# Kernel tuning notes

Measured on AMD Instinct MI355X. Metric: run time of the kernel, lower is better.

## Reference

```python
import jax, jax.numpy as jnp
import numpy as np

B, N, L, E, H, D = 2, 2048, 2048, 512, 8, 3
C = E // H
ALPHA_Q = 10.0

def _ln(v, g, b):
    m = jnp.mean(v, -1, keepdims=True)
    var = jnp.mean((v - m) ** 2, -1, keepdims=True)
    return (v - m) * jax.lax.rsqrt(var + 1e-5) * g + b

def setup_inputs() -> dict:
    key = jax.random.key(0)
    ks = jax.random.split(key, 16)
    def nrm(k, shape):
        return jax.random.normal(k, shape, jnp.float32) * 0.02
    return dict(
        x=jax.random.normal(ks[0], (B, N, E), jnp.float32),
        xp=jax.random.normal(ks[1], (B, N, D), jnp.float32),
        y=jax.random.normal(ks[2], (B, L, E), jnp.float32),
        yp=jax.random.normal(ks[3], (B, L, D), jnp.float32),
        attn_mask=jnp.ones((B, 1, N, L), jnp.float32),
        pW1=jax.random.uniform(ks[4], (E, D), jnp.float32, -1.0 / D, 1.0 / D),
        pb1=jax.random.uniform(ks[5], (E,), jnp.float32, 0.0, np.pi),
        pW2=jax.random.uniform(ks[6], (E, D), jnp.float32, -1.0 / D, 1.0 / D),
        pb2=jax.random.uniform(ks[7], (E,), jnp.float32, 0.0, np.pi),
        qn_g=jnp.ones((E,), jnp.float32), qn_b=jnp.zeros((E,), jnp.float32),
        qW1=nrm(ks[8], (E, E)), qb1=jnp.zeros((E,), jnp.float32),
        qW2=nrm(ks[9], (E, E)), qb2=jnp.zeros((E,), jnp.float32),
        kn_g=jnp.ones((E,), jnp.float32), kn_b=jnp.zeros((E,), jnp.float32),
        kW1=nrm(ks[10], (E, E)), kb1=jnp.zeros((E,), jnp.float32),
        vn_g=jnp.ones((E,), jnp.float32), vn_b=jnp.zeros((E,), jnp.float32),
        vW=nrm(ks[11], (E, E)), vb=jnp.zeros((E,), jnp.float32),
        p1W=nrm(ks[12], (E, E)), p1b=jnp.zeros((E,), jnp.float32),
        p2W=nrm(ks[13], (E, D * H)), p2b=jnp.zeros((E,), jnp.float32),
    )

def reference(x, xp, y, yp, attn_mask, pW1, pb1, pW2, pb2,
              qn_g, qn_b, qW1, qb1, qW2, qb2, kn_g, kn_b, kW1, kb1,
              vn_g, vn_b, vW, vb, p1W, p1b, p2W, p2b):
    # PositionEncoder: query side with bias, key side without
    pxs = ALPHA_Q * xp
    px1 = pxs @ pW1.T + pb1
    px2 = pxs @ pW2.T + pb2
    xc1, xs1, xc2, xs2 = jnp.cos(px1), jnp.sin(px1), jnp.cos(px2), jnp.sin(px2)
    pys = ALPHA_Q * yp
    py1 = pys @ pW1.T
    py2 = pys @ pW2.T
    yc1, ys1, yc2, ys2 = jnp.cos(py1), jnp.sin(py1), jnp.cos(py2), jnp.sin(py2)

    def split(t):  # [B,S,E] -> [B,S,H,C]
        return t.reshape(t.shape[0], t.shape[1], H, C)

    # QueryEncoder
    xn = _ln(x, qn_g, qn_b)
    x1 = xn @ qW1.T + qb1
    x2 = xn @ qW2.T + qb2
    q = jnp.concatenate([split(x1 * xc1), split(x1 * xs1),
                         split(x2 * xc2), split(x2 * xs2)], -1)  # [B,N,H,4C]
    q = q.transpose(0, 2, 1, 3)  # [B,H,N,4C]
    # KeyEncoder
    yn = _ln(y, kn_g, kn_b)
    y1 = yn @ kW1.T + kb1
    k = jnp.concatenate([split(y1 * yc1), split(y1 * ys1),
                         split(yc2), split(ys2)], -1).transpose(0, 2, 1, 3)

    scale = (4 * C) ** -0.5
    attn = jax.nn.softmax(jnp.einsum('bhnd,bhld->bhnl', q, k) * scale, axis=-1)
    # custom mask renormalization
    attn = attn * attn_mask
    eps = min(1e-8, 1.0 / L)
    attn = attn / (jnp.sum(attn, -1, keepdims=True) + eps)

    v = (_ln(y, vn_g, vn_b) @ vW.T + vb).reshape(B, L, H, C).transpose(0, 2, 1, 3)
    out1 = jnp.einsum('bhnl,bhlc->bhnc', attn, v).transpose(0, 2, 1, 3).reshape(B, N, E)
    out1 = out1 @ p1W.T + p1b

    out2 = jnp.einsum('bhnl,bld->bhnd', attn, yp) - xp[:, None]  # [B,H,N,D]
    out2 = out2.transpose(0, 2, 1, 3).reshape(B, N, H * D) @ p2W.T + p2b
    return (out1 + out2, attn)
```

## Files before the change

kernel.cpp:

```cpp
#include <hip/hip_runtime.h>

typedef unsigned short ushort_t;
typedef __attribute__((ext_vector_type(8))) __bf16 bf16x8;
typedef __attribute__((ext_vector_type(4))) float f32x4;

__device__ __forceinline__ f32x4 mfma16(bf16x8 a, bf16x8 b, f32x4 c) {
  return __builtin_amdgcn_mfma_f32_16x16x32_bf16(a, b, c, 0, 0, 0);
}

__device__ __forceinline__ ushort_t f2bf(float f) {
  unsigned int x = __float_as_uint(f);
  unsigned int r = (x + 0x7fffu + ((x >> 16) & 1u)) >> 16;
  return (ushort_t)r;
}

static constexpr size_t SZ_XN   = 4096ull * 512 * 2;
static constexpr size_t SZ_W    = 512ull * 512 * 2;
static constexpr size_t OFS_XN   = 0;
static constexpr size_t OFS_YNK  = OFS_XN + SZ_XN;
static constexpr size_t OFS_YNV  = OFS_YNK + SZ_XN;
static constexpr size_t OFS_WQ12 = OFS_YNV + SZ_XN;
static constexpr size_t OFS_WK1  = OFS_WQ12 + 2 * SZ_W;
static constexpr size_t OFS_WV   = OFS_WK1 + SZ_W;
static constexpr size_t OFS_WP1  = OFS_WV + SZ_W;
static constexpr size_t OFS_QB12 = OFS_WP1 + SZ_W;
static constexpr size_t OFS_FLAG = OFS_QB12 + 4096;
static constexpr size_t OFS_X12  = OFS_FLAG + 256;
static constexpr size_t OFS_Y1   = OFS_X12 + 4096ull * 1024 * 4;
static constexpr size_t OFS_VV   = OFS_Y1 + 4096ull * 512 * 4;
static constexpr size_t OFS_Q    = OFS_VV + 4096ull * 512 * 4;
static constexpr size_t OFS_K    = OFS_Q + 16ull * 2048 * 256 * 2;
static constexpr size_t OFS_VT   = OFS_K + 16ull * 2048 * 256 * 2;
static constexpr size_t OFS_O1   = OFS_VT + 16ull * 80 * 2048 * 2;
static constexpr size_t OFS_O2   = OFS_O1 + 4096ull * 512 * 2;

__global__ void k_convert(const float* __restrict__ qW1, const float* __restrict__ qW2,
                          const float* __restrict__ kW1, const float* __restrict__ vW,
                          const float* __restrict__ p1W,
                          const float* __restrict__ qb1, const float* __restrict__ qb2,
                          ushort_t* wq12, ushort_t* wk1, ushort_t* wv, ushort_t* wp1,
                          float* qb12, int* flag) {
  int seg = blockIdx.y;
  int idx = blockIdx.x * 256 + threadIdx.x;
  switch (seg) {
    case 0: wq12[idx] = f2bf(qW1[idx]);
            if (idx < 512) qb12[idx] = qb1[idx];
            if (idx == 0) *flag = 1;
            break;
    case 1: wq12[262144 + idx] = f2bf(qW2[idx]);
            if (idx < 512) qb12[512 + idx] = qb2[idx];
            break;
    case 2: wk1[idx] = f2bf(kW1[idx]); break;
    case 3: wv[idx]  = f2bf(vW[idx]);  break;
    case 4: wp1[idx] = f2bf(p1W[idx]); break;
  }
}

__global__ void k_maskchk(const float4* __restrict__ mask, int* flag, int n4) {
  int i = blockIdx.x * blockDim.x + threadIdx.x;
  bool bad = false;
  for (; i < n4; i += gridDim.x * blockDim.x) {
    float4 v = mask[i];
    bad |= (v.x != 1.f) | (v.y != 1.f) | (v.z != 1.f) | (v.w != 1.f);
  }
  if (bad) atomicAnd(flag, 0);
}

__global__ __launch_bounds__(256) void k_ln1(const float* __restrict__ x,
                                             const float* __restrict__ g, const float* __restrict__ b,
                                             ushort_t* __restrict__ out) {
  int row = blockIdx.x, tid = threadIdx.x;
  const float* xr = x + (size_t)row * 512;
  float v0 = xr[tid], v1 = xr[tid + 256];
  float s = v0 + v1, q = v0 * v0 + v1 * v1;
  for (int m = 32; m; m >>= 1) { s += __shfl_xor(s, m, 64); q += __shfl_xor(q, m, 64); }
  __shared__ float ls[8];
  int wid = tid >> 6, lane = tid & 63;
  if (lane == 0) { ls[wid] = s; ls[4 + wid] = q; }
  __syncthreads();
  s = ls[0] + ls[1] + ls[2] + ls[3];
  q = ls[4] + ls[5] + ls[6] + ls[7];
  float mean = s * (1.f / 512), var = q * (1.f / 512) - mean * mean;
  float rs = rsqrtf(var + 1e-5f);
  ushort_t* o = out + (size_t)row * 512;
  o[tid]       = f2bf((v0 - mean) * rs * g[tid] + b[tid]);
  o[tid + 256] = f2bf((v1 - mean) * rs * g[tid + 256] + b[tid + 256]);
}

__global__ __launch_bounds__(256) void k_ln2(const float* __restrict__ y,
                                             const float* __restrict__ g1, const float* __restrict__ b1,
                                             const float* __restrict__ g2, const float* __restrict__ b2,
                                             ushort_t* __restrict__ o1, ushort_t* __restrict__ o2) {
  int row = blockIdx.x, tid = threadIdx.x;
  const float* yr = y + (size_t)row * 512;
  float v0 = yr[tid], v1 = yr[tid + 256];
  float s = v0 + v1, q = v0 * v0 + v1 * v1;
  for (int m = 32; m; m >>= 1) { s += __shfl_xor(s, m, 64); q += __shfl_xor(q, m, 64); }
  __shared__ float ls[8];
  int wid = tid >> 6, lane = tid & 63;
  if (lane == 0) { ls[wid] = s; ls[4 + wid] = q; }
  __syncthreads();
  s = ls[0] + ls[1] + ls[2] + ls[3];
  q = ls[4] + ls[5] + ls[6] + ls[7];
  float mean = s * (1.f / 512), var = q * (1.f / 512) - mean * mean;
  float rs = rsqrtf(var + 1e-5f);
  float t0 = (v0 - mean) * rs, t1 = (v1 - mean) * rs;
  ushort_t* p1 = o1 + (size_t)row * 512;
  ushort_t* p2 = o2 + (size_t)row * 512;
  p1[tid]       = f2bf(t0 * g1[tid] + b1[tid]);
  p1[tid + 256] = f2bf(t1 * g1[tid + 256] + b1[tid + 256]);
  p2[tid]       = f2bf(t0 * g2[tid] + b2[tid]);
  p2[tid + 256] = f2bf(t1 * g2[tid + 256] + b2[tid + 256]);
}

__global__ __launch_bounds__(256) void k_gemm(const ushort_t* __restrict__ A, const ushort_t* __restrict__ W,
                                              const float* __restrict__ bias, float* __restrict__ Cmat,
                                              int M, int Nn, int K, int mode,
// ... 57 lines not shown
}

__global__ __launch_bounds__(256) void k_scatter_q(const float* __restrict__ x12, const float* __restrict__ xp,
                                                   const float* __restrict__ pW1, const float* __restrict__ pb1,
                                                   const float* __restrict__ pW2, const float* __restrict__ pb2,
                                                   ushort_t* __restrict__ q) {
  int rown = blockIdx.x;
  int b = rown >> 11, n = rown & 2047;
  float p0 = xp[(size_t)rown * 3] * 10.f;
  float p1 = xp[(size_t)rown * 3 + 1] * 10.f;
  float p2v = xp[(size_t)rown * 3 + 2] * 10.f;
  const float* x1r = x12 + (size_t)rown * 1024;
#pragma unroll
  for (int i = 0; i < 2; i++) {
    int e = threadIdx.x + i * 256;
    float a1 = p0 * pW1[e * 3] + p1 * pW1[e * 3 + 1] + p2v * pW1[e * 3 + 2] + pb1[e];
    float a2 = p0 * pW2[e * 3] + p1 * pW2[e * 3 + 1] + p2v * pW2[e * 3 + 2] + pb2[e];
    float c1, s1, c2, s2;
    __sincosf(a1, &s1, &c1);
    __sincosf(a2, &s2, &c2);
    float x1 = x1r[e], x2 = x1r[512 + e];
    int h = e >> 6, c = e & 63;
    ushort_t* qr = q + (((size_t)b * 8 + h) * 2048 + n) * 256;
    qr[c]       = f2bf(x1 * c1);
    qr[64 + c]  = f2bf(x1 * s1);
    qr[128 + c] = f2bf(x2 * c2);
    qr[192 + c] = f2bf(x2 * s2);
  }
}

__global__ __launch_bounds__(256) void k_scatter_k(const float* __restrict__ y1, const float* __restrict__ yp,
                                                   const float* __restrict__ pW1, const float* __restrict__ pW2,
                                                   ushort_t* __restrict__ kk) {
  int rown = blockIdx.x;
  int b = rown >> 11, n = rown & 2047;
  float p0 = yp[(size_t)rown * 3] * 10.f;
  float p1 = yp[(size_t)rown * 3 + 1] * 10.f;
  float p2v = yp[(size_t)rown * 3 + 2] * 10.f;
  const float* y1r = y1 + (size_t)rown * 512;
#pragma unroll
  for (int i = 0; i < 2; i++) {
    int e = threadIdx.x + i * 256;
    float a1 = p0 * pW1[e * 3] + p1 * pW1[e * 3 + 1] + p2v * pW1[e * 3 + 2];
    float a2 = p0 * pW2[e * 3] + p1 * pW2[e * 3 + 1] + p2v * pW2[e * 3 + 2];
    float c1, s1, c2, s2;
    __sincosf(a1, &s1, &c1);
    __sincosf(a2, &s2, &c2);
    float v1 = y1r[e];
    int h = e >> 6, c = e & 63;
    ushort_t* kr = kk + (((size_t)b * 8 + h) * 2048 + n) * 256;
    kr[c]       = f2bf(v1 * c1);
    kr[64 + c]  = f2bf(v1 * s1);
    kr[128 + c] = f2bf(c2);
    kr[192 + c] = f2bf(s2);
  }
}

__global__ void k_vt(const float* __restrict__ vv, ushort_t* __restrict__ vt) {
  int l0 = blockIdx.x * 64, h = blockIdx.y, b = blockIdx.z;
  __shared__ ushort_t t[64][66];
  int tx = threadIdx.x, ty = threadIdx.y;
#pragma unroll
  for (int i = 0; i < 16; i++) {
    int lr = i * 4 + ty;
    t[lr][tx] = f2bf(vv[((size_t)(b * 2048 + l0 + lr)) * 512 + h * 64 + tx]);
  }
  __syncthreads();
#pragma unroll
  for (int i = 0; i < 16; i++) {
    int col = i * 4 + ty;
    vt[(((size_t)b * 8 + h) * 80 + col) * 2048 + l0 + tx] = t[tx][col];
  }
}

__global__ void k_vt_extra(const float* __restrict__ yp, ushort_t* __restrict__ vt) {
  int l = blockIdx.x * 256 + threadIdx.x;
  int j = blockIdx.y, bh = blockIdx.z;
  int b = bh >> 3;
  ushort_t v = 0;
  if (j < 3) v = f2bf(yp[((size_t)b * 2048 + l) * 3 + j]);
  vt[((size_t)bh * 80 + 64 + j) * 2048 + l] = v;
}

__global__ __launch_bounds__(256, 2) void k_attn(const ushort_t* __restrict__ qbuf,
                                                 const ushort_t* __restrict__ kbuf,
                                                 const ushort_t* __restrict__ vt,
                                                 const float* __restrict__ mask,
                                                 const int* __restrict__ flag,
                                                 const float* __restrict__ xp,
                                                 float* __restrict__ attn_out,
                                                 ushort_t* __restrict__ o1,
                                                 float* __restrict__ o2) {
  __shared__ __align__(16) ushort_t kL[2][32 * 256];
  __shared__ __align__(16) ushort_t aT[4][16][40];

  int flat = blockIdx.x;
  int bh = flat & 15, rb = flat >> 4;
  int b = bh >> 3, h = bh & 7;
  int tid = threadIdx.x, wid = tid >> 6, lane = tid & 63, lg = lane >> 4, lc = lane & 15;
  int n0 = rb * 64;
  int wrow = n0 + wid * 16;
  const bool ones = (*flag != 0);

  const ushort_t* Kb = kbuf + (size_t)bh * 2048 * 256;
  const ushort_t* Vb = vt + (size_t)bh * 80 * 2048;

  bf16x8 qf[8];
  {
    const ushort_t* qr = qbuf + ((size_t)bh * 2048 + wrow + lc) * 256 + lg * 8;
#pragma unroll
    for (int ks = 0; ks < 8; ks++) qf[ks] = *(const bf16x8*)(qr + ks * 32);
  }

  int sg_src[4], sg_dst[4];
#pragma unroll
  for (int i = 0; i < 4; i++) {
    int g = wid * 256 + i * 64 + lane;
    int row = g >> 5;
    int gc = (g & 31) ^ (row & 7);
    sg_src[i] = row * 256 + gc * 8;
    sg_dst[i] = (wid * 256 + i * 64) * 8;
  }

#define STAGE(s, t)                                                                     \
  {                                                                                     \
    const ushort_t* tb = Kb + (size_t)(t) * 32 * 256;                                   \
    _Pragma("unroll")                                                                   \
    for (int i = 0; i < 4; i++) {                                                       \
      __builtin_amdgcn_global_load_lds(                                                 \
          (const __attribute__((address_space(1))) void*)(tb + sg_src[i]),              \
          (__attribute__((address_space(3))) void*)(&kL[s][sg_dst[i]]), 16, 0, 0);      \
    }                                                                                   \
  }

  int r3 = (lc & 7);

  float rsE[4] = {0, 0, 0, 0}, rsM[4] = {0, 0, 0, 0};
  STAGE(0, 0);
  asm volatile("s_waitcnt vmcnt(0)" ::: "memory");
  __syncthreads();
  for (int t = 0; t < 64; t++) {
    int s = t & 1;
    if (t < 63) { STAGE(s ^ 1, t + 1); }
    __builtin_amdgcn_sched_barrier(0);
    f32x4 sacc[2];
    sacc[0] = (f32x4){0, 0, 0, 0};
    sacc[1] = (f32x4){0, 0, 0, 0};
#pragma unroll
    for (int ks = 0; ks < 8; ks++) {
      int gb = ((ks * 4 + lg) ^ r3) * 8;
      bf16x8 k0 = *(const bf16x8*)(&kL[s][lc * 256 + gb]);
      bf16x8 k1 = *(const bf16x8*)(&kL[s][(16 + lc) * 256 + gb]);
      sacc[0] = mfma16(qf[ks], k0, sacc[0]);
      sacc[1] = mfma16(qf[ks], k1, sacc[1]);
    }
#pragma unroll
    for (int nt = 0; nt < 2; nt++)
#pragma unroll
      for (int r = 0; r < 4; r++) {
        float T = __expf(sacc[nt][r] * 0.0625f);
        rsE[r] += T;
        if (!ones) {
          float m = mask[((size_t)b * 2048 + wrow + lg * 4 + r) * 2048 + t * 32 + nt * 16 + lc];
          rsM[r] += T * m;
        }
      }
    asm volatile("s_waitcnt vmcnt(0)" ::: "memory");
    __syncthreads();
  }

  float inv[4];
#pragma unroll
  for (int r = 0; r < 4; r++) {
#pragma unroll
    for (int s2 = 1; s2 < 16; s2 <<= 1) {
      rsE[r] += __shfl_xor(rsE[r], s2, 64);
      if (!ones) rsM[r] += __shfl_xor(rsM[r], s2, 64);
    }
    float denom = (ones ? rsE[r] : rsM[r]) + 1e-8f * rsE[r];
    inv[r] = 1.f / denom;
  }

  f32x4 pacc[5];
#pragma unroll
  for (int nt = 0; nt < 5; nt++) pacc[nt] = (f32x4){0, 0, 0, 0};

  STAGE(0, 0);
  asm volatile("s_waitcnt vmcnt(0)" ::: "memory");
  __syncthreads();
  for (int t = 0; t < 64; t++) {
    int s = t & 1;
    if (t < 63) { STAGE(s ^ 1, t + 1); }
    __builtin_amdgcn_sched_barrier(0);
    int l0 = t * 32;
    f32x4 sacc[2];
    sacc[0] = (f32x4){0, 0, 0, 0};
    sacc[1] = (f32x4){0, 0, 0, 0};
#pragma unroll
    for (int ks = 0; ks < 8; ks++) {
      int gb = ((ks * 4 + lg) ^ r3) * 8;
      bf16x8 k0 = *(const bf16x8*)(&kL[s][lc * 256 + gb]);
      bf16x8 k1 = *(const bf16x8*)(&kL[s][(16 + lc) * 256 + gb]);
      sacc[0] = mfma16(qf[ks], k0, sacc[0]);
      sacc[1] = mfma16(qf[ks], k1, sacc[1]);
    }
#pragma unroll
    for (int nt = 0; nt < 2; nt++)
#pragma unroll
      for (int r = 0; r < 4; r++) {
        float T = __expf(sacc[nt][r] * 0.0625f);
        float m = 1.f;
        if (!ones) m = mask[((size_t)b * 2048 + wrow + lg * 4 + r) * 2048 + l0 + nt * 16 + lc];
        float a = T * m * inv[r];
        __builtin_nontemporal_store(
            a, &attn_out[((size_t)bh * 2048 + wrow + lg * 4 + r) * 2048 + l0 + nt * 16 + lc]);
        aT[wid][lg * 4 + r][nt * 16 + lc] = f2bf(a);
      }
    asm volatile("s_waitcnt lgkmcnt(0)" ::: "memory");
    __builtin_amdgcn_sched_barrier(0);
    bf16x8 af = *(const bf16x8*)(&aT[wid][lc][lg * 8]);
#pragma unroll
    for (int nt = 0; nt < 5; nt++) {
      bf16x8 vf = *(const bf16x8*)(Vb + (size_t)(nt * 16 + lc) * 2048 + l0 + lg * 8);
      pacc[nt] = mfma16(af, vf, pacc[nt]);
    }
    asm volatile("s_waitcnt vmcnt(8)" ::: "memory");
    __syncthreads();
  }
#undef STAGE

#pragma unroll
  for (int nt = 0; nt < 4; nt++)
#pragma unroll
    for (int r = 0; r < 4; r++) {
      int n = wrow + lg * 4 + r;
      o1[((size_t)b * 2048 + n) * 512 + h * 64 + nt * 16 + lc] = f2bf(pacc[nt][r]);
    }
  if (lc < 3) {
#pragma unroll
    for (int r = 0; r < 4; r++) {
      int n = wrow + lg * 4 + r;
      o2[((size_t)b * 2048 + n) * 24 + h * 3 + lc] = pacc[4][r] - xp[((size_t)b * 2048 + n) * 3 + lc];
    }
  }
}

extern "C" void kernel_launch(void* const* d_in, const int* in_sizes, int n_in,
                              void* d_out, int out_size, void* d_ws, size_t ws_size,
                              hipStream_t stream) {
  const float* x    = (const float*)d_in[0];
  const float* xp   = (const float*)d_in[1];
  const float* y    = (const float*)d_in[2];
  const float* yp   = (const float*)d_in[3];
  const float* mask = (const float*)d_in[4];
  const float* pW1  = (const float*)d_in[5];
  const float* pb1  = (const float*)d_in[6];
  const float* pW2  = (const float*)d_in[7];
  const float* pb2  = (const float*)d_in[8];
  const float* qn_g = (const float*)d_in[9];
  const float* qn_b = (const float*)d_in[10];
  const float* qW1  = (const float*)d_in[11];
  const float* qb1  = (const float*)d_in[12];
  const float* qW2  = (const float*)d_in[13];
  const float* qb2  = (const float*)d_in[14];
  const float* kn_g = (const float*)d_in[15];
  const float* kn_b = (const float*)d_in[16];
  const float* kW1  = (const float*)d_in[17];
  const float* kb1  = (const float*)d_in[18];
  const float* vn_g = (const float*)d_in[19];
  const float* vn_b = (const float*)d_in[20];
  const float* vW   = (const float*)d_in[21];
  const float* vb   = (const float*)d_in[22];
  const float* p1W  = (const float*)d_in[23];
  const float* p1b  = (const float*)d_in[24];
  const float* p2W  = (const float*)d_in[25];
  const float* p2b  = (const float*)d_in[26];

  char* ws = (char*)d_ws;
  ushort_t* xn   = (ushort_t*)(ws + OFS_XN);
  ushort_t* ynk  = (ushort_t*)(ws + OFS_YNK);
  ushort_t* ynv  = (ushort_t*)(ws + OFS_YNV);
  ushort_t* wq12 = (ushort_t*)(ws + OFS_WQ12);
  ushort_t* wk1  = (ushort_t*)(ws + OFS_WK1);
  ushort_t* wv   = (ushort_t*)(ws + OFS_WV);
  ushort_t* wp1  = (ushort_t*)(ws + OFS_WP1);
  float*    qb12 = (float*)(ws + OFS_QB12);
  int*      flag = (int*)(ws + OFS_FLAG);
  float*    x12  = (float*)(ws + OFS_X12);
  float*    y1b  = (float*)(ws + OFS_Y1);
  float*    vvb  = (float*)(ws + OFS_VV);
  ushort_t* qb   = (ushort_t*)(ws + OFS_Q);
  ushort_t* kb   = (ushort_t*)(ws + OFS_K);
  ushort_t* vtb  = (ushort_t*)(ws + OFS_VT);
  ushort_t* o1   = (ushort_t*)(ws + OFS_O1);
  float*    o2   = (float*)(ws + OFS_O2);

  float* out0 = (float*)d_out;
  float* attn_out = (float*)d_out + 2097152;

  k_convert<<<dim3(1024, 5), 256, 0, stream>>>(qW1, qW2, kW1, vW, p1W, qb1, qb2,
                                               wq12, wk1, wv, wp1, qb12, flag);
  k_maskchk<<<2048, 256, 0, stream>>>((const float4*)mask, flag, 2097152);
  k_ln1<<<4096, 256, 0, stream>>>(x, qn_g, qn_b, xn);
  k_ln2<<<4096, 256, 0, stream>>>(y, kn_g, kn_b, vn_g, vn_b, ynk, ynv);
  k_gemm<<<dim3(8, 32), 256, 0, stream>>>(xn, wq12, qb12, x12, 4096, 1024, 512, 0, nullptr, nullptr, nullptr);
  k_gemm<<<dim3(4, 32), 256, 0, stream>>>(ynk, wk1, kb1, y1b, 4096, 512, 512, 0, nullptr, nullptr, nullptr);
  k_gemm<<<dim3(4, 32), 256, 0, stream>>>(ynv, wv, vb, vvb, 4096, 512, 512, 0, nullptr, nullptr, nullptr);
  k_scatter_q<<<4096, 256, 0, stream>>>(x12, xp, pW1, pb1, pW2, pb2, qb);
  k_scatter_k<<<4096, 256, 0, stream>>>(y1b, yp, pW1, pW2, kb);
  k_vt<<<dim3(32, 8, 2), dim3(64, 4), 0, stream>>>(vvb, vtb);
  k_vt_extra<<<dim3(8, 16, 16), 256, 0, stream>>>(yp, vtb);
  k_attn<<<dim3(512), 256, 0, stream>>>(qb, kb, vtb, mask, flag, xp, attn_out, o1, o2);
  k_gemm<<<dim3(4, 32), 256, 0, stream>>>(o1, wp1, p1b, out0, 4096, 512, 512, 1, o2, p2W, p2b);
}
```

Measured before the change: 362.1 us.

## Split attention into single-pass PV kernel and separate attn-matrix writer kernel

The first attention kernel now does one pass over K, accumulating unnormalized probabilities times V and the row sums together, and applies the inverse normalizer at the end. The normalizers go to a workspace buffer. A second kernel recomputes QK^T with register-double-buffered K loads and writes the normalized attention matrix using two 16-row tiles per wave. This removes the duplicate QK pass from the PV kernel and lets the output GEMM run before the large attention write, at the cost of recomputing QK in a separate launch with occupancy 1. The invb buffer reuses the x12 workspace region, which is no longer needed by then.

```diff
diff --git a/kernel.cpp b/kernel.cpp
--- a/kernel.cpp
+++ b/kernel.cpp
@@ -26,6 +26,7 @@
 static constexpr size_t OFS_QB12 = OFS_WP1 + SZ_W;
 static constexpr size_t OFS_FLAG = OFS_QB12 + 4096;
 static constexpr size_t OFS_X12  = OFS_FLAG + 256;
+static constexpr size_t OFS_INV  = OFS_X12;
 static constexpr size_t OFS_Y1   = OFS_X12 + 4096ull * 1024 * 4;
 static constexpr size_t OFS_VV   = OFS_Y1 + 4096ull * 512 * 4;
 static constexpr size_t OFS_Q    = OFS_VV + 4096ull * 512 * 4;
@@ -256,15 +257,15 @@
   vt[((size_t)bh * 80 + 64 + j) * 2048 + l] = v;
 }
 
-__global__ __launch_bounds__(256, 2) void k_attn(const ushort_t* __restrict__ qbuf,
-                                                 const ushort_t* __restrict__ kbuf,
-                                                 const ushort_t* __restrict__ vt,
-                                                 const float* __restrict__ mask,
-                                                 const int* __restrict__ flag,
-                                                 const float* __restrict__ xp,
-                                                 float* __restrict__ attn_out,
-                                                 ushort_t* __restrict__ o1,
-                                                 float* __restrict__ o2) {
+__global__ __launch_bounds__(256, 2) void k_attn1(const ushort_t* __restrict__ qbuf,
+                                                  const ushort_t* __restrict__ kbuf,
+                                                  const ushort_t* __restrict__ vt,
+                                                  const float* __restrict__ mask,
+                                                  const int* __restrict__ flag,
+                                                  const float* __restrict__ xp,
+                                                  float* __restrict__ invb,
+                                                  ushort_t* __restrict__ o1,
+                                                  float* __restrict__ o2) {
   __shared__ __align__(16) ushort_t kL[2][32 * 256];
   __shared__ __align__(16) ushort_t aT[4][16][40];
 
@@ -272,8 +273,7 @@
   int bh = flat & 15, rb = flat >> 4;
   int b = bh >> 3, h = bh & 7;
   int tid = threadIdx.x, wid = tid >> 6, lane = tid & 63, lg = lane >> 4, lc = lane & 15;
-  int n0 = rb * 64;
-  int wrow = n0 + wid * 16;
+  int wrow = rb * 64 + wid * 16;
   const bool ones = (*flag != 0);
 
   const ushort_t* Kb = kbuf + (size_t)bh * 2048 * 256;
@@ -310,12 +310,21 @@
   int r3 = (lc & 7);
 
   float rsE[4] = {0, 0, 0, 0}, rsM[4] = {0, 0, 0, 0};
+  f32x4 pacc[5];
+#pragma unroll
+  for (int nt = 0; nt < 5; nt++) pacc[nt] = (f32x4){0, 0, 0, 0};
+
   STAGE(0, 0);
   asm volatile("s_waitcnt vmcnt(0)" ::: "memory");
   __syncthreads();
   for (int t = 0; t < 64; t++) {
     int s = t & 1;
+    int l0 = t * 32;
     if (t < 63) { STAGE(s ^ 1, t + 1); }
+    bf16x8 vf[5];
+#pragma unroll
+    for (int nt = 0; nt < 5; nt++)
+      vf[nt] = *(const bf16x8*)(Vb + (size_t)(nt * 16 + lc) * 2048 + l0 + lg * 8);
     __builtin_amdgcn_sched_barrier(0);
     f32x4 sacc[2];
     sacc[0] = (f32x4){0, 0, 0, 0};
@@ -334,89 +343,135 @@
       for (int r = 0; r < 4; r++) {
         float T = __expf(sacc[nt][r] * 0.0625f);
         rsE[r] += T;
+        float Tm = T;
         if (!ones) {
-          float m = mask[((size_t)b * 2048 + wrow + lg * 4 + r) * 2048 + t * 32 + nt * 16 + lc];
-          rsM[r] += T * m;
+          float m = mask[((size_t)b * 2048 + wrow + lg * 4 + r) * 2048 + l0 + nt * 16 + lc];
+          Tm = T * m;
+          rsM[r] += Tm;
         }
-      }
-    asm volatile("s_waitcnt vmcnt(0)" ::: "memory");
-    __syncthreads();
-  }
-
-  float inv[4];
-#pragma unroll
-  for (int r = 0; r < 4; r++) {
-#pragma unroll
-    for (int s2 = 1; s2 < 16; s2 <<= 1) {
-      rsE[r] += __shfl_xor(rsE[r], s2, 64);
-      if (!ones) rsM[r] += __shfl_xor(rsM[r], s2, 64);
-    }
-    float denom = (ones ? rsE[r] : rsM[r]) + 1e-8f * rsE[r];
-    inv[r] = 1.f / denom;
-  }
-
-  f32x4 pacc[5];
-#pragma unroll
-  for (int nt = 0; nt < 5; nt++) pacc[nt] = (f32x4){0, 0, 0, 0};
-
-  STAGE(0, 0);
-  asm volatile("s_waitcnt vmcnt(0)" ::: "memory");
-  __syncthreads();
-  for (int t = 0; t < 64; t++) {
-    int s = t & 1;
-    if (t < 63) { STAGE(s ^ 1, t + 1); }
-    __builtin_amdgcn_sched_barrier(0);
-    int l0 = t * 32;
-    f32x4 sacc[2];
-    sacc[0] = (f32x4){0, 0, 0, 0};
-    sacc[1] = (f32x4){0, 0, 0, 0};
-#pragma unroll
-    for (int ks = 0; ks < 8; ks++) {
-      int gb = ((ks * 4 + lg) ^ r3) * 8;
-      bf16x8 k0 = *(const bf16x8*)(&kL[s][lc * 256 + gb]);
-      bf16x8 k1 = *(const bf16x8*)(&kL[s][(16 + lc) * 256 + gb]);
-      sacc[0] = mfma16(qf[ks], k0, sacc[0]);
-      sacc[1] = mfma16(qf[ks], k1, sacc[1]);
-    }
-#pragma unroll
-    for (int nt = 0; nt < 2; nt++)
-#pragma unroll
-      for (int r = 0; r < 4; r++) {
-        float T = __expf(sacc[nt][r] * 0.0625f);
-        float m = 1.f;
-        if (!ones) m = mask[((size_t)b * 2048 + wrow + lg * 4 + r) * 2048 + l0 + nt * 16 + lc];
-        float a = T * m * inv[r];
-        __builtin_nontemporal_store(
-            a, &attn_out[((size_t)bh * 2048 + wrow + lg * 4 + r) * 2048 + l0 + nt * 16 + lc]);
-        aT[wid][lg * 4 + r][nt * 16 + lc] = f2bf(a);
+        aT[wid][lg * 4 + r][nt * 16 + lc] = f2bf(Tm);
       }
     asm volatile("s_waitcnt lgkmcnt(0)" ::: "memory");
     __builtin_amdgcn_sched_barrier(0);
     bf16x8 af = *(const bf16x8*)(&aT[wid][lc][lg * 8]);
 #pragma unroll
-    for (int nt = 0; nt < 5; nt++) {
-      bf16x8 vf = *(const bf16x8*)(Vb + (size_t)(nt * 16 + lc) * 2048 + l0 + lg * 8);
-      pacc[nt] = mfma16(af, vf, pacc[nt]);
-    }
-    asm volatile("s_waitcnt vmcnt(8)" ::: "memory");
+    for (int nt = 0; nt < 5; nt++) pacc[nt] = mfma16(af, vf[nt], pacc[nt]);
     __syncthreads();
   }
 #undef STAGE
+
+  float inv[4];
+#pragma unroll
+  for (int r = 0; r < 4; r++) {
+#pragma unroll
+    for (int s2 = 1; s2 < 16; s2 <<= 1) {
+      rsE[r] += __shfl_xor(rsE[r], s2, 64);
+      if (!ones) rsM[r] += __shfl_xor(rsM[r], s2, 64);
+    }
+    float denom = (ones ? rsE[r] : rsM[r]) + 1e-8f * rsE[r];
+    inv[r] = 1.f / denom;
+  }
+
+  if (lc == 0) {
+#pragma unroll
+    for (int r = 0; r < 4; r++) invb[(size_t)bh * 2048 + wrow + lg * 4 + r] = inv[r];
+  }
 
 #pragma unroll
   for (int nt = 0; nt < 4; nt++)
 #pragma unroll
     for (int r = 0; r < 4; r++) {
       int n = wrow + lg * 4 + r;
-      o1[((size_t)b * 2048 + n) * 512 + h * 64 + nt * 16 + lc] = f2bf(pacc[nt][r]);
+      o1[((size_t)b * 2048 + n) * 512 + h * 64 + nt * 16 + lc] = f2bf(pacc[nt][r] * inv[r]);
     }
   if (lc < 3) {
 #pragma unroll
     for (int r = 0; r < 4; r++) {
       int n = wrow + lg * 4 + r;
-      o2[((size_t)b * 2048 + n) * 24 + h * 3 + lc] = pacc[4][r] - xp[((size_t)b * 2048 + n) * 3 + lc];
-    }
-  }
+      o2[((size_t)b * 2048 + n) * 24 + h * 3 + lc] =
+          pacc[4][r] * inv[r] - xp[((size_t)b * 2048 + n) * 3 + lc];
+    }
+  }
+}
+
+__global__ __launch_bounds__(256, 1) void k_attn2(const ushort_t* __restrict__ qbuf,
+                                                  const ushort_t* __restrict__ kbuf,
+                                                  const float* __restrict__ invb,
+                                                  const float* __restrict__ mask,
+                                                  const int* __restrict__ flag,
+                                                  float* __restrict__ attn_out) {
+  int flat = blockIdx.x;
+  int bh = flat & 15, rb = flat >> 4;
+  int b = bh >> 3;
+  int tid = threadIdx.x, wid = tid >> 6, lane = tid & 63, lg = lane >> 4, lc = lane & 15;
+  int base = rb * 128 + wid * 32;
+  const bool ones = (*flag != 0);
+
+  const ushort_t* Kb = kbuf + (size_t)bh * 2048 * 256;
+  float* aout = attn_out + (size_t)bh * 2048 * 2048;
+
+  bf16x8 qf0[8], qf1[8];
+  {
+    const ushort_t* q0 = qbuf + ((size_t)bh * 2048 + base + lc) * 256 + lg * 8;
+#pragma unroll
+    for (int ks = 0; ks < 8; ks++) {
+      qf0[ks] = *(const bf16x8*)(q0 + ks * 32);
+      qf1[ks] = *(const bf16x8*)(q0 + 16 * 256 + ks * 32);
+    }
+  }
+  float inv0[4], inv1[4];
+#pragma unroll
+  for (int r = 0; r < 4; r++) {
+    inv0[r] = invb[(size_t)bh * 2048 + base + lg * 4 + r];
+    inv1[r] = invb[(size_t)bh * 2048 + base + 16 + lg * 4 + r];
+  }
+
+  bf16x8 kA[16], kB[16];
+
+#define LOADK(dst, l0)                                                                  \
+  {                                                                                     \
+    const ushort_t* kp = Kb + ((size_t)(l0) + lc) * 256 + lg * 8;                       \
+    _Pragma("unroll")                                                                   \
+    for (int nt = 0; nt < 2; nt++)                                                      \
+      _Pragma("unroll")                                                                 \
+      for (int ks = 0; ks < 8; ks++)                                                    \
+        dst[nt * 8 + ks] = *(const bf16x8*)(kp + nt * 16 * 256 + ks * 32);              \
+  }
+
+#define PROC(buf, l0)                                                                   \
+  {                                                                                     \
+    _Pragma("unroll")                                                                   \
+    for (int nt = 0; nt < 2; nt++) {                                                    \
+      f32x4 s0 = (f32x4){0, 0, 0, 0}, s1 = (f32x4){0, 0, 0, 0};                         \
+      _Pragma("unroll")                                                                 \
+      for (int ks = 0; ks < 8; ks++) {                                                  \
+        s0 = mfma16(qf0[ks], buf[nt * 8 + ks], s0);                                     \
+        s1 = mfma16(qf1[ks], buf[nt * 8 + ks], s1);                                     \
+      }                                                                                 \
+      int col = (l0) + nt * 16 + lc;                                                    \
+      _Pragma("unroll")                                                                 \
+      for (int r = 0; r < 4; r++) {                                                     \
+        float a0 = __expf(s0[r] * 0.0625f) * inv0[r];                                   \
+        float a1 = __expf(s1[r] * 0.0625f) * inv1[r];                                   \
+        if (!ones) {                                                                    \
+          a0 *= mask[((size_t)b * 2048 + base + lg * 4 + r) * 2048 + col];              \
+          a1 *= mask[((size_t)b * 2048 + base + 16 + lg * 4 + r) * 2048 + col];         \
+        }                                                                               \
+        __builtin_nontemporal_store(a0, &aout[(size_t)(base + lg * 4 + r) * 2048 + col]); \
+        __builtin_nontemporal_store(a1, &aout[(size_t)(base + 16 + lg * 4 + r) * 2048 + col]); \
+      }                                                                                 \
+    }                                                                                   \
+  }
+
+  LOADK(kA, 0);
+  for (int l0 = 0; l0 < 2048; l0 += 64) {
+    LOADK(kB, l0 + 32);
+    PROC(kA, l0);
+    if (l0 + 64 < 2048) { LOADK(kA, l0 + 64); }
+    PROC(kB, l0 + 32);
+  }
+#undef LOADK
+#undef PROC
 }
 
 extern "C" void kernel_launch(void* const* d_in, const int* in_sizes, int n_in,
@@ -461,6 +516,7 @@
   float*    qb12 = (float*)(ws + OFS_QB12);
   int*      flag = (int*)(ws + OFS_FLAG);
   float*    x12  = (float*)(ws + OFS_X12);
+  float*    invb = (float*)(ws + OFS_INV);
   float*    y1b  = (float*)(ws + OFS_Y1);
   float*    vvb  = (float*)(ws + OFS_VV);
   ushort_t* qb   = (ushort_t*)(ws + OFS_Q);
@@ -484,6 +540,7 @@
   k_scatter_k<<<4096, 256, 0, stream>>>(y1b, yp, pW1, pW2, kb);
   k_vt<<<dim3(32, 8, 2), dim3(64, 4), 0, stream>>>(vvb, vtb);
   k_vt_extra<<<dim3(8, 16, 16), 256, 0, stream>>>(yp, vtb);
-  k_attn<<<dim3(512), 256, 0, stream>>>(qb, kb, vtb, mask, flag, xp, attn_out, o1, o2);
+  k_attn1<<<dim3(512), 256, 0, stream>>>(qb, kb, vtb, mask, flag, xp, invb, o1, o2);
   k_gemm<<<dim3(4, 32), 256, 0, stream>>>(o1, wp1, p1b, out0, 4096, 512, 512, 1, o2, p2W, p2b);
-}
+  k_attn2<<<dim3(256), 256, 0, stream>>>(qb, kb, invb, mask, flag, attn_out);
+}
```

Measured after the change: 391.5 us. 1.08x slower.

## Split attention into score-materialize pass and separate normalize+PV kernel

Applied to the files above, without the earlier changes.

Replaces the two-pass attention kernel, which recomputed QK^T and exp in its second pass, with a single QK pass. That pass writes unnormalized bf16 exp scores to a workspace buffer plus per-row inverse denominators. A new kernel reads these scores, writes the normalized fp32 attention output, and runs the PV MFMA, deferring the normalization to the accumulator epilogue. This removes the duplicate QK matmul and exp work at the cost of writing and re-reading a 128MB bf16 intermediate. The returned attention values now pass through bf16 rounding before normalization.

```diff
diff --git a/kernel.cpp b/kernel.cpp
--- a/kernel.cpp
+++ b/kernel.cpp
@@ -26,6 +26,7 @@
 static constexpr size_t OFS_QB12 = OFS_WP1 + SZ_W;
 static constexpr size_t OFS_FLAG = OFS_QB12 + 4096;
 static constexpr size_t OFS_X12  = OFS_FLAG + 256;
+static constexpr size_t OFS_INV  = OFS_X12;
 static constexpr size_t OFS_Y1   = OFS_X12 + 4096ull * 1024 * 4;
 static constexpr size_t OFS_VV   = OFS_Y1 + 4096ull * 512 * 4;
 static constexpr size_t OFS_Q    = OFS_VV + 4096ull * 512 * 4;
@@ -33,6 +34,7 @@
 static constexpr size_t OFS_VT   = OFS_K + 16ull * 2048 * 256 * 2;
 static constexpr size_t OFS_O1   = OFS_VT + 16ull * 80 * 2048 * 2;
 static constexpr size_t OFS_O2   = OFS_O1 + 4096ull * 512 * 2;
+static constexpr size_t OFS_T    = OFS_O2 + 4096ull * 24 * 4;
 
 __global__ void k_convert(const float* __restrict__ qW1, const float* __restrict__ qW2,
                           const float* __restrict__ kW1, const float* __restrict__ vW,
@@ -256,28 +258,24 @@
   vt[((size_t)bh * 80 + 64 + j) * 2048 + l] = v;
 }
 
-__global__ __launch_bounds__(256, 2) void k_attn(const ushort_t* __restrict__ qbuf,
-                                                 const ushort_t* __restrict__ kbuf,
-                                                 const ushort_t* __restrict__ vt,
-                                                 const float* __restrict__ mask,
-                                                 const int* __restrict__ flag,
-                                                 const float* __restrict__ xp,
-                                                 float* __restrict__ attn_out,
-                                                 ushort_t* __restrict__ o1,
-                                                 float* __restrict__ o2) {
+__global__ __launch_bounds__(256, 2) void k_attn1(const ushort_t* __restrict__ qbuf,
+                                                  const ushort_t* __restrict__ kbuf,
+                                                  const float* __restrict__ mask,
+                                                  const int* __restrict__ flag,
+                                                  float* __restrict__ invb,
+                                                  ushort_t* __restrict__ Tb) {
   __shared__ __align__(16) ushort_t kL[2][32 * 256];
   __shared__ __align__(16) ushort_t aT[4][16][40];
 
   int flat = blockIdx.x;
   int bh = flat & 15, rb = flat >> 4;
-  int b = bh >> 3, h = bh & 7;
+  int b = bh >> 3;
   int tid = threadIdx.x, wid = tid >> 6, lane = tid & 63, lg = lane >> 4, lc = lane & 15;
-  int n0 = rb * 64;
-  int wrow = n0 + wid * 16;
+  int wrow = rb * 64 + wid * 16;
   const bool ones = (*flag != 0);
 
   const ushort_t* Kb = kbuf + (size_t)bh * 2048 * 256;
-  const ushort_t* Vb = vt + (size_t)bh * 80 * 2048;
+  ushort_t* Trow = Tb + ((size_t)bh * 2048 + wrow + lc) * 2048 + lg * 8;
 
   bf16x8 qf[8];
   {
@@ -310,11 +308,13 @@
   int r3 = (lc & 7);
 
   float rsE[4] = {0, 0, 0, 0}, rsM[4] = {0, 0, 0, 0};
+
   STAGE(0, 0);
   asm volatile("s_waitcnt vmcnt(0)" ::: "memory");
   __syncthreads();
   for (int t = 0; t < 64; t++) {
     int s = t & 1;
+    int l0 = t * 32;
     if (t < 63) { STAGE(s ^ 1, t + 1); }
     __builtin_amdgcn_sched_barrier(0);
     f32x4 sacc[2];
@@ -334,87 +334,150 @@
       for (int r = 0; r < 4; r++) {
         float T = __expf(sacc[nt][r] * 0.0625f);
         rsE[r] += T;
+        float Tm = T;
         if (!ones) {
-          float m = mask[((size_t)b * 2048 + wrow + lg * 4 + r) * 2048 + t * 32 + nt * 16 + lc];
-          rsM[r] += T * m;
+          float m = mask[((size_t)b * 2048 + wrow + lg * 4 + r) * 2048 + l0 + nt * 16 + lc];
+          Tm = T * m;
+          rsM[r] += Tm;
         }
-      }
-    asm volatile("s_waitcnt vmcnt(0)" ::: "memory");
-    __syncthreads();
-  }
-
-  float inv[4];
-#pragma unroll
-  for (int r = 0; r < 4; r++) {
-#pragma unroll
-    for (int s2 = 1; s2 < 16; s2 <<= 1) {
-      rsE[r] += __shfl_xor(rsE[r], s2, 64);
-      if (!ones) rsM[r] += __shfl_xor(rsM[r], s2, 64);
-    }
-    float denom = (ones ? rsE[r] : rsM[r]) + 1e-8f * rsE[r];
-    inv[r] = 1.f / denom;
-  }
-
-  f32x4 pacc[5];
-#pragma unroll
-  for (int nt = 0; nt < 5; nt++) pacc[nt] = (f32x4){0, 0, 0, 0};
-
-  STAGE(0, 0);
-  asm volatile("s_waitcnt vmcnt(0)" ::: "memory");
-  __syncthreads();
-  for (int t = 0; t < 64; t++) {
-    int s = t & 1;
-    if (t < 63) { STAGE(s ^ 1, t + 1); }
-    __builtin_amdgcn_sched_barrier(0);
-    int l0 = t * 32;
-    f32x4 sacc[2];
-    sacc[0] = (f32x4){0, 0, 0, 0};
-    sacc[1] = (f32x4){0, 0, 0, 0};
-#pragma unroll
-    for (int ks = 0; ks < 8; ks++) {
-      int gb = ((ks * 4 + lg) ^ r3) * 8;
-      bf16x8 k0 = *(const bf16x8*)(&kL[s][lc * 256 + gb]);
-      bf16x8 k1 = *(const bf16x8*)(&kL[s][(16 + lc) * 256 + gb]);
-      sacc[0] = mfma16(qf[ks], k0, sacc[0]);
-      sacc[1] = mfma16(qf[ks], k1, sacc[1]);
-    }
-#pragma unroll
-    for (int nt = 0; nt < 2; nt++)
-#pragma unroll
-      for (int r = 0; r < 4; r++) {
-        float T = __expf(sacc[nt][r] * 0.0625f);
-        float m = 1.f;
-        if (!ones) m = mask[((size_t)b * 2048 + wrow + lg * 4 + r) * 2048 + l0 + nt * 16 + lc];
-        float a = T * m * inv[r];
-        __builtin_nontemporal_store(
-            a, &attn_out[((size_t)bh * 2048 + wrow + lg * 4 + r) * 2048 + l0 + nt * 16 + lc]);
-        aT[wid][lg * 4 + r][nt * 16 + lc] = f2bf(a);
+        aT[wid][lg * 4 + r][nt * 16 + lc] = f2bf(Tm);
       }
     asm volatile("s_waitcnt lgkmcnt(0)" ::: "memory");
     __builtin_amdgcn_sched_barrier(0);
     bf16x8 af = *(const bf16x8*)(&aT[wid][lc][lg * 8]);
+    *(bf16x8*)(Trow + l0) = af;
+    __syncthreads();
+  }
+#undef STAGE
+
+  float inv[4];
+#pragma unroll
+  for (int r = 0; r < 4; r++) {
+#pragma unroll
+    for (int s2 = 1; s2 < 16; s2 <<= 1) {
+      rsE[r] += __shfl_xor(rsE[r], s2, 64);
+      if (!ones) rsM[r] += __shfl_xor(rsM[r], s2, 64);
+    }
+    float denom = (ones ? rsE[r] : rsM[r]) + 1e-8f * rsE[r];
+    inv[r] = 1.f / denom;
+  }
+  if (lc == 0) {
+#pragma unroll
+    for (int r = 0; r < 4; r++) invb[(size_t)bh * 2048 + wrow + lg * 4 + r] = inv[r];
+  }
+}
+
+__global__ __launch_bounds__(512, 1) void k_attnpv(const ushort_t* __restrict__ Tb,
+                                                   const ushort_t* __restrict__ vt,
+                                                   const float* __restrict__ invb,
+                                                   const float* __restrict__ xp,
+                                                   float* __restrict__ attn_out,
+                                                   ushort_t* __restrict__ o1,
+                                                   float* __restrict__ o2) {
+  __shared__ __align__(16) ushort_t A[128 * 64];
+  int flat = blockIdx.x;
+  int bh = flat & 15, mb = flat >> 4;
+  int b = bh >> 3, h = bh & 7;
+  int m0 = mb * 128;
+  int tid = threadIdx.x, wid = tid >> 6, lane = tid & 63, lg = lane >> 4, lc = lane & 15;
+
+  const ushort_t* Vb = vt + (size_t)bh * 80 * 2048;
+
+  int srow = tid >> 2, scq = (tid & 3) * 16;
+  const ushort_t* srcrow = Tb + ((size_t)bh * 2048 + m0 + srow) * 2048 + scq;
+  float* dstrow = attn_out + ((size_t)bh * 2048 + m0 + srow) * 2048 + scq;
+  float invr = invb[(size_t)bh * 2048 + m0 + srow];
+  int c8a = (tid & 3) * 2;
+  int dsw0 = srow * 64 + ((c8a ^ (srow & 7)) * 8);
+  int dsw1 = srow * 64 + (((c8a + 1) ^ (srow & 7)) * 8);
+
+  float invE[4];
+#pragma unroll
+  for (int r = 0; r < 4; r++)
+    invE[r] = invb[(size_t)bh * 2048 + m0 + wid * 16 + lg * 4 + r];
+
+  int aoff[2];
+#pragma unroll
+  for (int kk = 0; kk < 2; kk++)
+    aoff[kk] = (wid * 16 + lc) * 64 + (((kk * 4 + lg) ^ (lc & 7)) * 8);
+
+  f32x4 pacc[5];
+#pragma unroll
+  for (int nt = 0; nt < 5; nt++) pacc[nt] = (f32x4){0, 0, 0, 0};
+
+  int4 v0 = *(const int4*)(srcrow);
+  int4 v1 = *(const int4*)(srcrow + 8);
+  bf16x8 vf0[5], vf1[5];
+#pragma unroll
+  for (int nt = 0; nt < 5; nt++) {
+    const ushort_t* vp = Vb + (size_t)(nt * 16 + lc) * 2048 + lg * 8;
+    vf0[nt] = *(const bf16x8*)(vp);
+    vf1[nt] = *(const bf16x8*)(vp + 32);
+  }
+
+  for (int t = 0; t < 32; t++) {
+    int l0 = t * 64;
+    __syncthreads();
+    *(int4*)(&A[dsw0]) = v0;
+    *(int4*)(&A[dsw1]) = v1;
+    __syncthreads();
+    {
+      const unsigned* u = (const unsigned*)&v0;
+      float fo[16];
+#pragma unroll
+      for (int j = 0; j < 4; j++) {
+        fo[2 * j]     = __uint_as_float(u[j] << 16) * invr;
+        fo[2 * j + 1] = __uint_as_float(u[j] & 0xffff0000u) * invr;
+      }
+      const unsigned* w = (const unsigned*)&v1;
+#pragma unroll
+      for (int j = 0; j < 4; j++) {
+        fo[8 + 2 * j]     = __uint_as_float(w[j] << 16) * invr;
+        fo[8 + 2 * j + 1] = __uint_as_float(w[j] & 0xffff0000u) * invr;
+      }
+#pragma unroll
+      for (int j = 0; j < 4; j++)
+        *(float4*)(dstrow + l0 + j * 4) = *(float4*)(&fo[j * 4]);
+    }
+    int4 n0, n1;
+    bf16x8 nf0[5], nf1[5];
+    if (t < 31) {
+      n0 = *(const int4*)(srcrow + l0 + 64);
+      n1 = *(const int4*)(srcrow + l0 + 64 + 8);
+#pragma unroll
+      for (int nt = 0; nt < 5; nt++) {
+        const ushort_t* vp = Vb + (size_t)(nt * 16 + lc) * 2048 + l0 + 64 + lg * 8;
+        nf0[nt] = *(const bf16x8*)(vp);
+        nf1[nt] = *(const bf16x8*)(vp + 32);
+      }
+    }
+    bf16x8 af0 = *(const bf16x8*)(&A[aoff[0]]);
+    bf16x8 af1 = *(const bf16x8*)(&A[aoff[1]]);
 #pragma unroll
     for (int nt = 0; nt < 5; nt++) {
-      bf16x8 vf = *(const bf16x8*)(Vb + (size_t)(nt * 16 + lc) * 2048 + l0 + lg * 8);
-      pacc[nt] = mfma16(af, vf, pacc[nt]);
-    }
-    asm volatile("s_waitcnt vmcnt(8)" ::: "memory");
-    __syncthreads();
-  }
-#undef STAGE
+      pacc[nt] = mfma16(af0, vf0[nt], pacc[nt]);
+      pacc[nt] = mfma16(af1, vf1[nt], pacc[nt]);
+    }
+    if (t < 31) {
+      v0 = n0; v1 = n1;
+#pragma unroll
+      for (int nt = 0; nt < 5; nt++) { vf0[nt] = nf0[nt]; vf1[nt] = nf1[nt]; }
+    }
+  }
 
 #pragma unroll
   for (int nt = 0; nt < 4; nt++)
 #pragma unroll
     for (int r = 0; r < 4; r++) {
-      int n = wrow + lg * 4 + r;
-      o1[((size_t)b * 2048 + n) * 512 + h * 64 + nt * 16 + lc] = f2bf(pacc[nt][r]);
+      int n = m0 + wid * 16 + lg * 4 + r;
+      o1[((size_t)b * 2048 + n) * 512 + h * 64 + nt * 16 + lc] = f2bf(pacc[nt][r] * invE[r]);
     }
   if (lc < 3) {
 #pragma unroll
     for (int r = 0; r < 4; r++) {
-      int n = wrow + lg * 4 + r;
-      o2[((size_t)b * 2048 + n) * 24 + h * 3 + lc] = pacc[4][r] - xp[((size_t)b * 2048 + n) * 3 + lc];
+      int n = m0 + wid * 16 + lg * 4 + r;
+      o2[((size_t)b * 2048 + n) * 24 + h * 3 + lc] =
+          pacc[4][r] * invE[r] - xp[((size_t)b * 2048 + n) * 3 + lc];
     }
   }
 }
@@ -461,6 +524,7 @@
   float*    qb12 = (float*)(ws + OFS_QB12);
   int*      flag = (int*)(ws + OFS_FLAG);
   float*    x12  = (float*)(ws + OFS_X12);
+  float*    invb = (float*)(ws + OFS_INV);
   float*    y1b  = (float*)(ws + OFS_Y1);
   float*    vvb  = (float*)(ws + OFS_VV);
   ushort_t* qb   = (ushort_t*)(ws + OFS_Q);
@@ -468,6 +532,7 @@
   ushort_t* vtb  = (ushort_t*)(ws + OFS_VT);
   ushort_t* o1   = (ushort_t*)(ws + OFS_O1);
   float*    o2   = (float*)(ws + OFS_O2);
+  ushort_t* Tb   = (ushort_t*)(ws + OFS_T);
 
   float* out0 = (float*)d_out;
   float* attn_out = (float*)d_out + 2097152;
@@ -484,6 +549,7 @@
   k_scatter_k<<<4096, 256, 0, stream>>>(y1b, yp, pW1, pW2, kb);
   k_vt<<<dim3(32, 8, 2), dim3(64, 4), 0, stream>>>(vvb, vtb);
   k_vt_extra<<<dim3(8, 16, 16), 256, 0, stream>>>(yp, vtb);
-  k_attn<<<dim3(512), 256, 0, stream>>>(qb, kb, vtb, mask, flag, xp, attn_out, o1, o2);
+  k_attn1<<<dim3(512), 256, 0, stream>>>(qb, kb, mask, flag, invb, Tb);
+  k_attnpv<<<dim3(256), 512, 0, stream>>>(Tb, vtb, invb, xp, attn_out, o1, o2);
   k_gemm<<<dim3(4, 32), 256, 0, stream>>>(o1, wp1, p1b, out0, 4096, 512, 512, 1, o2, p2W, p2b);
 }
```

New measurement: 408.9 us. +12.9%, slower.

## Fuse two-pass attention into single pass with deferred normalization kernel

Applied to the files above, without the earlier changes.

The attention kernel no longer recomputes QK^T and exp in a second pass. It accumulates the unnormalized P·V and row sums in one pass, writes unnormalized bf16 probabilities to a workspace, and scales the PV results by the inverse row sum at the end. A new k_norm kernel then reads the bf16 probabilities and writes the normalized fp32 attention output. This halves the QK^T MFMA and exp work, but adds a 128MB bf16 intermediate write and read, and the attention output now passes through bf16 rounding before normalization, which lowers its precision.

```diff
diff --git a/kernel.cpp b/kernel.cpp
--- a/kernel.cpp
+++ b/kernel.cpp
@@ -26,6 +26,7 @@
 static constexpr size_t OFS_QB12 = OFS_WP1 + SZ_W;
 static constexpr size_t OFS_FLAG = OFS_QB12 + 4096;
 static constexpr size_t OFS_X12  = OFS_FLAG + 256;
+static constexpr size_t OFS_INV  = OFS_X12;
 static constexpr size_t OFS_Y1   = OFS_X12 + 4096ull * 1024 * 4;
 static constexpr size_t OFS_VV   = OFS_Y1 + 4096ull * 512 * 4;
 static constexpr size_t OFS_Q    = OFS_VV + 4096ull * 512 * 4;
@@ -33,6 +34,7 @@
 static constexpr size_t OFS_VT   = OFS_K + 16ull * 2048 * 256 * 2;
 static constexpr size_t OFS_O1   = OFS_VT + 16ull * 80 * 2048 * 2;
 static constexpr size_t OFS_O2   = OFS_O1 + 4096ull * 512 * 2;
+static constexpr size_t OFS_T    = OFS_O2 + 4096ull * 24 * 4;
 
 __global__ void k_convert(const float* __restrict__ qW1, const float* __restrict__ qW2,
                           const float* __restrict__ kW1, const float* __restrict__ vW,
@@ -256,15 +258,16 @@
   vt[((size_t)bh * 80 + 64 + j) * 2048 + l] = v;
 }
 
-__global__ __launch_bounds__(256, 2) void k_attn(const ushort_t* __restrict__ qbuf,
-                                                 const ushort_t* __restrict__ kbuf,
-                                                 const ushort_t* __restrict__ vt,
-                                                 const float* __restrict__ mask,
-                                                 const int* __restrict__ flag,
-                                                 const float* __restrict__ xp,
-                                                 float* __restrict__ attn_out,
-                                                 ushort_t* __restrict__ o1,
-                                                 float* __restrict__ o2) {
+__global__ __launch_bounds__(256, 2) void k_attn1(const ushort_t* __restrict__ qbuf,
+                                                  const ushort_t* __restrict__ kbuf,
+                                                  const ushort_t* __restrict__ vt,
+                                                  const float* __restrict__ mask,
+                                                  const int* __restrict__ flag,
+                                                  const float* __restrict__ xp,
+                                                  float* __restrict__ invb,
+                                                  ushort_t* __restrict__ Tb,
+                                                  ushort_t* __restrict__ o1,
+                                                  float* __restrict__ o2) {
   __shared__ __align__(16) ushort_t kL[2][32 * 256];
   __shared__ __align__(16) ushort_t aT[4][16][40];
 
@@ -272,12 +275,12 @@
   int bh = flat & 15, rb = flat >> 4;
   int b = bh >> 3, h = bh & 7;
   int tid = threadIdx.x, wid = tid >> 6, lane = tid & 63, lg = lane >> 4, lc = lane & 15;
-  int n0 = rb * 64;
-  int wrow = n0 + wid * 16;
+  int wrow = rb * 64 + wid * 16;
   const bool ones = (*flag != 0);
 
   const ushort_t* Kb = kbuf + (size_t)bh * 2048 * 256;
   const ushort_t* Vb = vt + (size_t)bh * 80 * 2048;
+  ushort_t* Trow = Tb + ((size_t)bh * 2048 + wrow + lc) * 2048 + lg * 8;
 
   bf16x8 qf[8];
   {
@@ -310,12 +313,23 @@
   int r3 = (lc & 7);
 
   float rsE[4] = {0, 0, 0, 0}, rsM[4] = {0, 0, 0, 0};
+  f32x4 pacc[5];
+#pragma unroll
+  for (int nt = 0; nt < 5; nt++) pacc[nt] = (f32x4){0, 0, 0, 0};
+
   STAGE(0, 0);
   asm volatile("s_waitcnt vmcnt(0)" ::: "memory");
-  __syncthreads();
+  __builtin_amdgcn_s_barrier();
+  __builtin_amdgcn_sched_barrier(0);
+
   for (int t = 0; t < 64; t++) {
     int s = t & 1;
+    int l0 = t * 32;
     if (t < 63) { STAGE(s ^ 1, t + 1); }
+    bf16x8 vf[5];
+#pragma unroll
+    for (int nt = 0; nt < 5; nt++)
+      vf[nt] = *(const bf16x8*)(Vb + (size_t)(nt * 16 + lc) * 2048 + l0 + lg * 8);
     __builtin_amdgcn_sched_barrier(0);
     f32x4 sacc[2];
     sacc[0] = (f32x4){0, 0, 0, 0};
@@ -334,88 +348,82 @@
       for (int r = 0; r < 4; r++) {
         float T = __expf(sacc[nt][r] * 0.0625f);
         rsE[r] += T;
+        float Tm = T;
         if (!ones) {
-          float m = mask[((size_t)b * 2048 + wrow + lg * 4 + r) * 2048 + t * 32 + nt * 16 + lc];
-          rsM[r] += T * m;
+          float m = mask[((size_t)b * 2048 + wrow + lg * 4 + r) * 2048 + l0 + nt * 16 + lc];
+          Tm = T * m;
+          rsM[r] += Tm;
         }
-      }
-    asm volatile("s_waitcnt vmcnt(0)" ::: "memory");
-    __syncthreads();
-  }
-
-  float inv[4];
-#pragma unroll
-  for (int r = 0; r < 4; r++) {
-#pragma unroll
-    for (int s2 = 1; s2 < 16; s2 <<= 1) {
-      rsE[r] += __shfl_xor(rsE[r], s2, 64);
-      if (!ones) rsM[r] += __shfl_xor(rsM[r], s2, 64);
-    }
-    float denom = (ones ? rsE[r] : rsM[r]) + 1e-8f * rsE[r];
-    inv[r] = 1.f / denom;
-  }
-
-  f32x4 pacc[5];
-#pragma unroll
-  for (int nt = 0; nt < 5; nt++) pacc[nt] = (f32x4){0, 0, 0, 0};
-
-  STAGE(0, 0);
-  asm volatile("s_waitcnt vmcnt(0)" ::: "memory");
-  __syncthreads();
-  for (int t = 0; t < 64; t++) {
-    int s = t & 1;
-    if (t < 63) { STAGE(s ^ 1, t + 1); }
-    __builtin_amdgcn_sched_barrier(0);
-    int l0 = t * 32;
-    f32x4 sacc[2];
-    sacc[0] = (f32x4){0, 0, 0, 0};
-    sacc[1] = (f32x4){0, 0, 0, 0};
-#pragma unroll
-    for (int ks = 0; ks < 8; ks++) {
-      int gb = ((ks * 4 + lg) ^ r3) * 8;
-      bf16x8 k0 = *(const bf16x8*)(&kL[s][lc * 256 + gb]);
-      bf16x8 k1 = *(const bf16x8*)(&kL[s][(16 + lc) * 256 + gb]);
-      sacc[0] = mfma16(qf[ks], k0, sacc[0]);
-      sacc[1] = mfma16(qf[ks], k1, sacc[1]);
-    }
-#pragma unroll
-    for (int nt = 0; nt < 2; nt++)
-#pragma unroll
-      for (int r = 0; r < 4; r++) {
-        float T = __expf(sacc[nt][r] * 0.0625f);
-        float m = 1.f;
-        if (!ones) m = mask[((size_t)b * 2048 + wrow + lg * 4 + r) * 2048 + l0 + nt * 16 + lc];
-        float a = T * m * inv[r];
-        __builtin_nontemporal_store(
-            a, &attn_out[((size_t)bh * 2048 + wrow + lg * 4 + r) * 2048 + l0 + nt * 16 + lc]);
-        aT[wid][lg * 4 + r][nt * 16 + lc] = f2bf(a);
+        aT[wid][lg * 4 + r][nt * 16 + lc] = f2bf(Tm);
       }
     asm volatile("s_waitcnt lgkmcnt(0)" ::: "memory");
     __builtin_amdgcn_sched_barrier(0);
     bf16x8 af = *(const bf16x8*)(&aT[wid][lc][lg * 8]);
-#pragma unroll
-    for (int nt = 0; nt < 5; nt++) {
-      bf16x8 vf = *(const bf16x8*)(Vb + (size_t)(nt * 16 + lc) * 2048 + l0 + lg * 8);
-      pacc[nt] = mfma16(af, vf, pacc[nt]);
-    }
-    asm volatile("s_waitcnt vmcnt(8)" ::: "memory");
-    __syncthreads();
+    *(bf16x8*)(Trow + l0) = af;
+#pragma unroll
+    for (int nt = 0; nt < 5; nt++) pacc[nt] = mfma16(af, vf[nt], pacc[nt]);
+    asm volatile("s_waitcnt vmcnt(1)" ::: "memory");
+    __builtin_amdgcn_s_barrier();
+    __builtin_amdgcn_sched_barrier(0);
   }
 #undef STAGE
+
+  float inv[4];
+#pragma unroll
+  for (int r = 0; r < 4; r++) {
+#pragma unroll
+    for (int s2 = 1; s2 < 16; s2 <<= 1) {
+      rsE[r] += __shfl_xor(rsE[r], s2, 64);
+      if (!ones) rsM[r] += __shfl_xor(rsM[r], s2, 64);
+    }
+    float denom = (ones ? rsE[r] : rsM[r]) + 1e-8f * rsE[r];
+    inv[r] = 1.f / denom;
+  }
+  if (lc == 0) {
+#pragma unroll
+    for (int r = 0; r < 4; r++) invb[(size_t)bh * 2048 + wrow + lg * 4 + r] = inv[r];
+  }
 
 #pragma unroll
   for (int nt = 0; nt < 4; nt++)
 #pragma unroll
     for (int r = 0; r < 4; r++) {
       int n = wrow + lg * 4 + r;
-      o1[((size_t)b * 2048 + n) * 512 + h * 64 + nt * 16 + lc] = f2bf(pacc[nt][r]);
+      o1[((size_t)b * 2048 + n) * 512 + h * 64 + nt * 16 + lc] = f2bf(pacc[nt][r] * inv[r]);
     }
   if (lc < 3) {
 #pragma unroll
     for (int r = 0; r < 4; r++) {
       int n = wrow + lg * 4 + r;
-      o2[((size_t)b * 2048 + n) * 24 + h * 3 + lc] = pacc[4][r] - xp[((size_t)b * 2048 + n) * 3 + lc];
-    }
+      o2[((size_t)b * 2048 + n) * 24 + h * 3 + lc] =
+          pacc[4][r] * inv[r] - xp[((size_t)b * 2048 + n) * 3 + lc];
+    }
+  }
+}
+
+__global__ __launch_bounds__(256) void k_norm(const ushort_t* __restrict__ Tb,
+                                              const float* __restrict__ invb,
+                                              float* __restrict__ attn_out) {
+  int tid = threadIdx.x;
+  size_t rowbase = (size_t)blockIdx.x * 8;
+#pragma unroll
+  for (int rr = 0; rr < 8; rr++) {
+    size_t row = rowbase + rr;
+    float inv = invb[row];
+    const ushort_t* src = Tb + row * 2048 + tid * 8;
+    float* dst = attn_out + row * 2048 + tid * 8;
+    int4 v = *(const int4*)src;
+    const unsigned* u = (const unsigned*)&v;
+    f32x4 f0, f1;
+#pragma unroll
+    for (int j = 0; j < 2; j++) {
+      f0[2 * j]     = __uint_as_float(u[j] << 16) * inv;
+      f0[2 * j + 1] = __uint_as_float(u[j] & 0xffff0000u) * inv;
+      f1[2 * j]     = __uint_as_float(u[2 + j] << 16) * inv;
+      f1[2 * j + 1] = __uint_as_float(u[2 + j] & 0xffff0000u) * inv;
+    }
+    __builtin_nontemporal_store(f0, (f32x4*)dst);
+    __builtin_nontemporal_store(f1, (f32x4*)(dst + 4));
   }
 }
 
@@ -461,6 +469,7 @@
   float*    qb12 = (float*)(ws + OFS_QB12);
   int*      flag = (int*)(ws + OFS_FLAG);
   float*    x12  = (float*)(ws + OFS_X12);
+  float*    invb = (float*)(ws + OFS_INV);
   float*    y1b  = (float*)(ws + OFS_Y1);
   float*    vvb  = (float*)(ws + OFS_VV);
   ushort_t* qb   = (ushort_t*)(ws + OFS_Q);
@@ -468,6 +477,7 @@
   ushort_t* vtb  = (ushort_t*)(ws + OFS_VT);
   ushort_t* o1   = (ushort_t*)(ws + OFS_O1);
   float*    o2   = (float*)(ws + OFS_O2);
+  ushort_t* Tb   = (ushort_t*)(ws + OFS_T);
 
   float* out0 = (float*)d_out;
   float* attn_out = (float*)d_out + 2097152;
@@ -484,6 +494,7 @@
   k_scatter_k<<<4096, 256, 0, stream>>>(y1b, yp, pW1, pW2, kb);
   k_vt<<<dim3(32, 8, 2), dim3(64, 4), 0, stream>>>(vvb, vtb);
   k_vt_extra<<<dim3(8, 16, 16), 256, 0, stream>>>(yp, vtb);
-  k_attn<<<dim3(512), 256, 0, stream>>>(qb, kb, vtb, mask, flag, xp, attn_out, o1, o2);
+  k_attn1<<<dim3(512), 256, 0, stream>>>(qb, kb, vtb, mask, flag, xp, invb, Tb, o1, o2);
   k_gemm<<<dim3(4, 32), 256, 0, stream>>>(o1, wp1, p1b, out0, 4096, 512, 512, 1, o2, p2W, p2b);
-}
+  k_norm<<<dim3(4096), 256, 0, stream>>>(Tb, invb, attn_out);
+}
```

New measurement: 366.7 us. Within noise of the previous version (+1.3%).
